# Optimization experiments

Hardware: AMD Instinct MI355X
Metric: run time of the kernel (lower is better)

The kernel has to match this reference:

```python
import jax, jax.numpy as jnp
import numpy as np

TOP_K = 9  # ATSSMatcher default


def setup_inputs() -> dict:
    key = jax.random.key(0)
    k1, k2, k3, k4 = jax.random.split(key, 4)
    N, M = 120000, 800
    IMG = 1024.0
    # anchors: valid x1<x2, y1<y2 boxes
    a_ctr = jax.random.uniform(k1, (N, 2)) * IMG
    a_sz = jax.random.uniform(k2, (N, 2)) * 60.0 + 8.0
    anchors = jnp.concatenate([a_ctr - a_sz / 2, a_ctr + a_sz / 2], axis=1)
    g_ctr = jax.random.uniform(k3, (M, 2)) * IMG
    g_sz = jax.random.uniform(k4, (M, 2)) * 100.0 + 10.0
    gt_boxes = jnp.concatenate([g_ctr - g_sz / 2, g_ctr + g_sz / 2], axis=1)
    return {"anchors": anchors, "gt_boxes": gt_boxes}


def _box_iou(a, b):
    # a: [N,4], b: [M,4] -> [N,M]
    area_a = (a[:, 2] - a[:, 0]) * (a[:, 3] - a[:, 1])
    area_b = (b[:, 2] - b[:, 0]) * (b[:, 3] - b[:, 1])
    lt = jnp.maximum(a[:, None, :2], b[None, :, :2])
    rb = jnp.minimum(a[:, None, 2:], b[None, :, 2:])
    wh = jnp.clip(rb - lt, 0.0)
    inter = wh[..., 0] * wh[..., 1]
    union = area_a[:, None] + area_b[None, :] - inter
    return inter / jnp.maximum(union, 1e-12)


def reference(anchors, gt_boxes):
    N = anchors.shape[0]
    M = gt_boxes.shape[0]
    ious = _box_iou(anchors, gt_boxes)                         # [N, M]
    a_ctr = (anchors[:, :2] + anchors[:, 2:]) / 2              # [N, 2]
    g_ctr = (gt_boxes[:, :2] + gt_boxes[:, 2:]) / 2            # [M, 2]
    # center distances [M, N] (per-GT rows for top-k along last axis)
    d = jnp.linalg.norm(a_ctr[None, :, :] - g_ctr[:, None, :], axis=-1)
    _, topk_idx = jax.lax.top_k(-d, TOP_K)                     # [M, TOP_K] nearest anchors
    topk_ious = jnp.take_along_axis(ious.T, topk_idx, axis=1)  # [M, TOP_K]
    iou_mean = topk_ious.mean(axis=1)                          # [M]
    iou_std = jnp.std(topk_ious, axis=1, ddof=1)               # torch .std() is unbiased
    thresh = iou_mean + iou_std                                # [M]
    candidate = ious >= thresh[None, :]                        # [N, M]
    cx, cy = a_ctr[:, 0], a_ctr[:, 1]
    inside = ((cx[:, None] >= gt_boxes[None, :, 0]) &
              (cx[:, None] <= gt_boxes[None, :, 2]) &
              (cy[:, None] >= gt_boxes[None, :, 1]) &
              (cy[:, None] <= gt_boxes[None, :, 3]))           # [N, M]
    pos = candidate & inside                                   # [N, M]
    gt_ids = jnp.arange(M, dtype=jnp.int32)[None, :]
    matched_idxs = jnp.max(jnp.where(pos, gt_ids, -1), axis=1)  # [N]
    gathered = jnp.take_along_axis(
        ious, jnp.clip(matched_idxs, 0)[:, None].astype(jnp.int32), axis=1)[:, 0]
    max_ious = jnp.where(matched_idxs >= 0, gathered, 0.0)
    return matched_idxs.astype(jnp.int64), max_ious
```

## Files before the change

kernel.cpp:

```cpp
#include <hip/hip_runtime.h>
#include <stdint.h>

typedef unsigned int u32;
typedef unsigned long long u64;

#define TOPK 9
#define GA 64
#define CELL_A 16.0f
#define NCA (GA * GA)
#define GG 16
#define CELL_G 64.0f
#define NCG (GG * GG)
#define CAPA 96
#define CAPG 160
#define OVA 8192
#define OVG 1024

__global__ __launch_bounds__(256) void zero_counts(u32* __restrict__ p, int n)
{
    int i = blockIdx.x * 256 + threadIdx.x;
    if (i < n) p[i] = 0u;
}

__global__ __launch_bounds__(256) void bucket_insert(
    const float4* __restrict__ a4, const float4* __restrict__ g4,
    u32* __restrict__ cursA, u32* __restrict__ cursG, u32* __restrict__ ovfCnt,
    float2* __restrict__ bkCtr, u32* __restrict__ bkIdx,
    u32* __restrict__ gtBkt,
    u32* __restrict__ ovAidx, float2* __restrict__ ovActr,
    u32* __restrict__ ovGidx, int N, int M)
{
    int gid = blockIdx.x * 256 + threadIdx.x;
    if (gid < N) {
        float4 a = a4[gid];
        float cx = (a.x + a.z) * 0.5f;
        float cy = (a.y + a.w) * 0.5f;
        int ix = min(GA - 1, max(0, (int)(cx * (1.0f / CELL_A))));
        int iy = min(GA - 1, max(0, (int)(cy * (1.0f / CELL_A))));
        int cell = iy * GA + ix;
        u32 p = atomicAdd(&cursA[cell], 1u);
        if (p < CAPA) {
            bkCtr[cell * CAPA + p] = make_float2(cx, cy);
            bkIdx[cell * CAPA + p] = (u32)gid;
        } else {
            u32 q = atomicAdd(&ovfCnt[0], 1u);
            if (q < OVA) { ovAidx[q] = (u32)gid; ovActr[q] = make_float2(cx, cy); }
        }
    } else if (gid < N + M) {
        int m = gid - N;
        float4 g = g4[m];
        int ix0 = min(GG - 1, max(0, (int)floorf(g.x * (1.0f / CELL_G))));
        int iy0 = min(GG - 1, max(0, (int)floorf(g.y * (1.0f / CELL_G))));
        int ix1 = min(GG - 1, max(0, (int)floorf(g.z * (1.0f / CELL_G))));
        int iy1 = min(GG - 1, max(0, (int)floorf(g.w * (1.0f / CELL_G))));
        for (int j = iy0; j <= iy1; ++j)
            for (int i = ix0; i <= ix1; ++i) {
                int cell = j * GG + i;
                u32 p = atomicAdd(&cursG[cell], 1u);
                if (p < CAPG) gtBkt[cell * CAPG + p] = (u32)m;
                else {
                    u32 q = atomicAdd(&ovfCnt[1], 1u);
                    if (q < OVG) ovGidx[q] = (u32)m;
                }
            }
    }
}

__global__ __launch_bounds__(256) void atss_query(
    const float4* __restrict__ a4, const float* __restrict__ gts,
    const u32* __restrict__ cursA, const float2* __restrict__ bkCtr,
    const u32* __restrict__ bkIdx, const u32* __restrict__ ovfCnt,
    const u32* __restrict__ ovAidx, const float2* __restrict__ ovActr,
    float* __restrict__ thresh, int N, int M)
{
    const int wid  = threadIdx.x >> 6;
    const int lane = threadIdx.x & 63;
    const int m = blockIdx.x * 4 + wid;
    if (m >= M) return;

    const float gx0 = gts[m * 4 + 0], gy0 = gts[m * 4 + 1];
    const float gx1 = gts[m * 4 + 2], gy1 = gts[m * 4 + 3];
    const float gcx = (gx0 + gx1) * 0.5f;
    const float gcy = (gy0 + gy1) * 0.5f;
    const int ci = min(GA - 1, max(0, (int)(gcx * (1.0f / CELL_A))));
    const int cj = min(GA - 1, max(0, (int)(gcy * (1.0f / CELL_A))));

    u32 cum = 0;
    float maxd2 = 0.f;
    for (int r = 0; r < GA && cum < TOPK; ++r) {
        int ncell = (r == 0) ? 1 : 8 * r;
        u32 myc = 0;
        float mymax = 0.f;
        for (int k = lane; k < ncell; k += 64) {
            int di = 0, dj = 0;
            if (r > 0) {
                int side = k / (2 * r), pos = k % (2 * r);
                if (side == 0)      { di = -r + pos; dj = -r; }
                else if (side == 1) { di = r;        dj = -r + pos; }
                else if (side == 2) { di = r - pos;  dj = r; }
                else                { di = -r;       dj = r - pos; }
            }
            int i = ci + di, j = cj + dj;
            if (i < 0 || i >= GA || j < 0 || j >= GA) continue;
            u32 cnt = cursA[j * GA + i];
            if (cnt) {
                myc += cnt;
                float x0 = i * CELL_A, x1 = x0 + CELL_A;
                float y0 = j * CELL_A, y1 = y0 + CELL_A;
                float dxm = fmaxf(gcx - x0, x1 - gcx);
                float dym = fmaxf(gcy - y0, y1 - gcy);
                mymax = fmaxf(mymax, dxm * dxm + dym * dym);
            }
        }
#pragma unroll
        for (int s2 = 1; s2 <= 32; s2 <<= 1) {
            myc += __shfl_xor(myc, s2, 64);
            mymax = fmaxf(mymax, __shfl_xor(mymax, s2, 64));
        }
        cum += myc;
        maxd2 = fmaxf(maxd2, mymax);
    }
    const float D2pad = maxd2 * 1.0001f + 1.0f;

    u64 kk[TOPK];
#pragma unroll
    for (int i = 0; i < TOPK; ++i) kk[i] = ~0ULL;

    const int rs = 1 + (int)(sqrtf(D2pad) * (1.0f / CELL_A));
    const int jlo = max(0, cj - rs), jhi = min(GA - 1, cj + rs);
    const int ilo = max(0, ci - rs), ihi = min(GA - 1, ci + rs);
    for (int j = jlo; j <= jhi; ++j) {
        float y0 = j * CELL_A, y1 = y0 + CELL_A;
        float mdy = fmaxf(fmaxf(y0 - gcy, gcy - y1), 0.f);
        for (int i = ilo; i <= ihi; ++i) {
            float x0 = i * CELL_A, x1 = x0 + CELL_A;
            float mdx = fmaxf(fmaxf(x0 - gcx, gcx - x1), 0.f);
            if (mdx * mdx + mdy * mdy > D2pad) continue;
            int c = j * GA + i;
            u32 cnt = min(cursA[c], (u32)CAPA);
            u32 base = (u32)c * CAPA;
            for (u32 tc = lane; tc < cnt; tc += 64) {
                u32 n = bkIdx[base + tc];
                float2 cc = bkCtr[base + tc];
                float ddx = cc.x - gcx, ddy = cc.y - gcy;
                float d2 = ddx * ddx + ddy * ddy;
                if (d2 <= D2pad) {
                    float d = sqrtf(d2);
                    u64 key = ((u64)__float_as_uint(d) << 32) | n;
                    if (key < kk[TOPK - 1]) {
                        u64 t2 = key;
#pragma unroll
                        for (int q = 0; q < TOPK; ++q) {
                            u64 lo = (kk[q] < t2) ? kk[q] : t2;
                            u64 hi = (kk[q] < t2) ? t2 : kk[q];
                            kk[q] = lo;
                            t2 = hi;
                        }
                    }
                }
            }
        }
    }
    {
        u32 nov = min(ovfCnt[0], (u32)OVA);
        for (u32 tc = lane; tc < nov; tc += 64) {
            u32 n = ovAidx[tc];
            float2 cc = ovActr[tc];
            float ddx = cc.x - gcx, ddy = cc.y - gcy;
            float d2 = ddx * ddx + ddy * ddy;
            if (d2 <= D2pad) {
                float d = sqrtf(d2);
                u64 key = ((u64)__float_as_uint(d) << 32) | n;
                if (key < kk[TOPK - 1]) {
                    u64 t2 = key;
#pragma unroll
                    for (int q = 0; q < TOPK; ++q) {
                        u64 lo = (kk[q] < t2) ? kk[q] : t2;
                        u64 hi = (kk[q] < t2) ? t2 : kk[q];
                        kk[q] = lo;
                        t2 = hi;
                    }
                }
            }
        }
    }

    u64 wins[TOPK];
#pragma unroll
    for (int rd = 0; rd < TOPK; ++rd) {
        u64 w = kk[0];
#pragma unroll
        for (int s2 = 1; s2 <= 32; s2 <<= 1) {
            u64 o = __shfl_xor(w, s2, 64);
            if (o < w) w = o;
        }
        wins[rd] = w;
        if (kk[0] == w) {
#pragma unroll
            for (int q = 0; q < TOPK - 1; ++q) kk[q] = kk[q + 1];
            kk[TOPK - 1] = ~0ULL;
        }
    }

    if (lane == 0) {
        const float area_g = (gx1 - gx0) * (gy1 - gy0);
        float vals[TOPK];
        float sum = 0.f;
#pragma unroll
        for (int r = 0; r < TOPK; ++r) {
            int idx = (int)(u32)(wins[r] & 0xffffffffULL);
            float4 a = a4[idx];
            float area_a = (a.z - a.x) * (a.w - a.y);
            float ltx = fmaxf(a.x, gx0), lty = fmaxf(a.y, gy0);
            float rbx = fminf(a.z, gx1), rby = fminf(a.w, gy1);
            float w2 = fmaxf(rbx - ltx, 0.f);
            float h2 = fmaxf(rby - lty, 0.f);
            float inter = w2 * h2;
            float uni = area_a + area_g - inter;
            float iou = inter / fmaxf(uni, 1e-12f);
            vals[r] = iou;
            sum += iou;
        }
        float mean = sum / 9.0f;
        float var = 0.f;
#pragma unroll
        for (int r = 0; r < TOPK; ++r) {
            float d2 = vals[r] - mean;
            var += d2 * d2;
        }
        float sd = sqrtf(var / 8.0f);
        thresh[m] = mean + sd;
    }
}

__global__ __launch_bounds__(256) void atss_assign(
    const float4* __restrict__ a4, const float4* __restrict__ g4,
    const float* __restrict__ thresh,
    const u32* __restrict__ cursG, const u32* __restrict__ gtBkt,
    const u32* __restrict__ ovfCnt, const u32* __restrict__ ovGidx,
    float* __restrict__ out_idx, float* __restrict__ out_iou, int N, int M)
{
    int n = blockIdx.x * 256 + threadIdx.x;
    if (n >= N) return;

    float4 a = a4[n];
    float area_a = (a.z - a.x) * (a.w - a.y);
    float cx = (a.x + a.z) * 0.5f;
    float cy = (a.y + a.w) * 0.5f;

    int ig = min(GG - 1, max(0, (int)(cx * (1.0f / CELL_G))));
    int jg = min(GG - 1, max(0, (int)(cy * (1.0f / CELL_G))));
    int cell = jg * GG + ig;

    u64 best = 0;
    u32 cnt = min(cursG[cell], (u32)CAPG);
    u32 base = (u32)cell * CAPG;
    for (u32 t2 = 0; t2 < cnt; ++t2) {
        int mi = (int)gtBkt[base + t2];
        float4 g = g4[mi];
        if (cx >= g.x && cx <= g.z && cy >= g.y && cy <= g.w) {
            float area_g = (g.z - g.x) * (g.w - g.y);
            float ltx = fmaxf(a.x, g.x), lty = fmaxf(a.y, g.y);
            float rbx = fminf(a.z, g.z), rby = fminf(a.w, g.w);
            float w = fmaxf(rbx - ltx, 0.f);
            float h = fmaxf(rby - lty, 0.f);
            float inter = w * h;
            float uni = area_a + area_g - inter;
            float iou = inter / fmaxf(uni, 1e-12f);
            if (iou >= thresh[mi]) {
                u64 cand = ((u64)(u32)(mi + 1) << 32) | __float_as_uint(iou);
                if (cand > best) best = cand;
            }
        }
    }
    {
        u32 nog = min(ovfCnt[1], (u32)OVG);
        for (u32 t2 = 0; t2 < nog; ++t2) {
            int mi = (int)ovGidx[t2];
            float4 g = g4[mi];
            if (cx >= g.x && cx <= g.z && cy >= g.y && cy <= g.w) {
                float area_g = (g.z - g.x) * (g.w - g.y);
                float ltx = fmaxf(a.x, g.x), lty = fmaxf(a.y, g.y);
                float rbx = fminf(a.z, g.z), rby = fminf(a.w, g.w);
                float w = fmaxf(rbx - ltx, 0.f);
                float h = fmaxf(rby - lty, 0.f);
                float inter = w * h;
                float uni = area_a + area_g - inter;
                float iou = inter / fmaxf(uni, 1e-12f);
                if (iou >= thresh[mi]) {
                    u64 cand = ((u64)(u32)(mi + 1) << 32) | __float_as_uint(iou);
                    if (cand > best) best = cand;
                }
            }
        }
    }

    int mm = (int)(best >> 32) - 1;
    out_idx[n] = (float)mm;
    out_iou[n] = (mm >= 0) ? __uint_as_float((u32)best) : 0.f;
}

__global__ __launch_bounds__(256) void fb_centers(
    const float4* __restrict__ a4, float2* __restrict__ c2, int N)
{
    int n = blockIdx.x * 256 + threadIdx.x;
    if (n < N) {
        float4 a = a4[n];
        c2[n] = make_float2((a.x + a.z) * 0.5f, (a.y + a.w) * 0.5f);
    }
}

__global__ __launch_bounds__(256) void fb_thresh(
    const float4* __restrict__ a4, const float2* __restrict__ c2,
    const float* __restrict__ gts, float* __restrict__ thresh, int N)
{
    const int m = blockIdx.x;
    const int tid = threadIdx.x;
    const float gx0 = gts[m * 4 + 0], gy0 = gts[m * 4 + 1];
    const float gx1 = gts[m * 4 + 2], gy1 = gts[m * 4 + 3];
    const float gcx = (gx0 + gx1) * 0.5f;
    const float gcy = (gy0 + gy1) * 0.5f;

    float vmin = __builtin_inff();
    for (int n = tid; n < N; n += 512) {
        float2 c = c2[n];
        float dx = c.x - gcx, dy = c.y - gcy;
        vmin = fminf(vmin, dx * dx + dy * dy);
    }
    float v = vmin, w = 0.f;
#pragma unroll
    for (int r = 0; r < TOPK; ++r) {
        float t = v;
#pragma unroll
        for (int s = 1; s <= 32; s <<= 1) t = fminf(t, __shfl_xor(t, s, 64));
        w = t;
        if (v == w) v = __builtin_inff();
    }
    const float T = sqrtf(w) * 1.0001f + 1e-6f;

    u64 k[TOPK];
#pragma unroll
    for (int i = 0; i < TOPK; ++i) k[i] = ~0ULL;
    for (int n = tid; n < N; n += 256) {
        float2 c = c2[n];
        float dx = c.x - gcx, dy = c.y - gcy;
        float d = sqrtf(dx * dx + dy * dy);
        if (d <= T) {
            u64 key = ((u64)__float_as_uint(d) << 32) | (unsigned)n;
            if (key < k[TOPK - 1]) {
                u64 t = key;
#pragma unroll
                for (int i = 0; i < TOPK; ++i) {
                    u64 lo = (k[i] < t) ? k[i] : t;
                    u64 hi = (k[i] < t) ? t : k[i];
                    k[i] = lo;
                    t = hi;
                }
            }
        }
    }
    __shared__ u64 red[256];
    __shared__ int top9[TOPK];
#pragma unroll 1
    for (int r = 0; r < TOPK; ++r) {
        red[tid] = k[0];
        __syncthreads();
        for (int s = 128; s > 0; s >>= 1) {
            if (tid < s) {
                u64 o = red[tid + s];
                if (o < red[tid]) red[tid] = o;
            }
            __syncthreads();
        }
        u64 win = red[0];
        if (tid == 0) top9[r] = (int)(unsigned)(win & 0xffffffffULL);
        __syncthreads();
        if (k[0] == win) {
#pragma unroll
            for (int i = 0; i < TOPK - 1; ++i) k[i] = k[i + 1];
            k[TOPK - 1] = ~0ULL;
        }
    }
    if (tid == 0) {
        const float area_g = (gx1 - gx0) * (gy1 - gy0);
        float vals[TOPK];
        float s = 0.f;
#pragma unroll
        for (int r = 0; r < TOPK; ++r) {
            float4 a = a4[top9[r]];
            float area_a = (a.z - a.x) * (a.w - a.y);
            float ltx = fmaxf(a.x, gx0), lty = fmaxf(a.y, gy0);
            float rbx = fminf(a.z, gx1), rby = fminf(a.w, gy1);
            float w2 = fmaxf(rbx - ltx, 0.f);
            float h2 = fmaxf(rby - lty, 0.f);
            float inter = w2 * h2;
            float uni = area_a + area_g - inter;
            float iou = inter / fmaxf(uni, 1e-12f);
            vals[r] = iou;
            s += iou;
        }
        float mean = s / 9.0f;
        float var = 0.f;
#pragma unroll
        for (int r = 0; r < TOPK; ++r) {
            float d2 = vals[r] - mean;
            var += d2 * d2;
        }
        thresh[m] = mean + sqrtf(var / 8.0f);
    }
}

__global__ __launch_bounds__(256) void fb_assign(
    const float4* __restrict__ a4, const float4* __restrict__ g4,
    const float* __restrict__ thresh,
    float* __restrict__ out_idx, float* __restrict__ out_iou, int N, int M)
{
    extern __shared__ char smem[];
    float4* sg = (float4*)smem;
    float2* se = (float2*)(smem + (size_t)M * 16);
    for (int i = threadIdx.x; i < M; i += 256) {
        float4 g = g4[i];
        sg[i] = g;
        se[i] = make_float2((g.z - g.x) * (g.w - g.y), thresh[i]);
    }
    __syncthreads();
    int n = blockIdx.x * 256 + threadIdx.x;
    if (n >= N) return;
    float4 a = a4[n];
    float area_a = (a.z - a.x) * (a.w - a.y);
    float cx = (a.x + a.z) * 0.5f;
    float cy = (a.y + a.w) * 0.5f;
    u64 best = 0;
    for (int mi = 0; mi < M; ++mi) {
        float4 g = sg[mi];
        if (cx >= g.x && cx <= g.z && cy >= g.y && cy <= g.w) {
            float2 e = se[mi];
            float ltx = fmaxf(a.x, g.x), lty = fmaxf(a.y, g.y);
            float rbx = fminf(a.z, g.z), rby = fminf(a.w, g.w);
            float w = fmaxf(rbx - ltx, 0.f);
            float h = fmaxf(rby - lty, 0.f);
            float inter = w * h;
            float uni = area_a + e.x - inter;
            float iou = inter / fmaxf(uni, 1e-12f);
            if (iou >= e.y)
                best = ((u64)(u32)(mi + 1) << 32) | __float_as_uint(iou);
        }
    }
    int mm = (int)(best >> 32) - 1;
    out_idx[n] = (float)mm;
    out_iou[n] = (mm >= 0) ? __uint_as_float((u32)best) : 0.f;
}

extern "C" void kernel_launch(void* const* d_in, const int* in_sizes, int n_in,
                              void* d_out, int out_size, void* d_ws, size_t ws_size,
                              hipStream_t stream) {
    const float4* a4 = (const float4*)d_in[0];
    const float4* g4 = (const float4*)d_in[1];
    const float* gts = (const float*)d_in[1];
    const int N = in_sizes[0] / 4;
    const int M = in_sizes[1] / 4;

    const size_t oCursA  = 0;
    const size_t oCursG  = oCursA + NCA;
    const size_t oOvfCnt = oCursG + NCG;
    const size_t oThresh = oOvfCnt + 2;
    size_t oBkCtr = oThresh + (size_t)M;
    oBkCtr = (oBkCtr + 1) & ~(size_t)1;
    const size_t oBkIdx  = oBkCtr + 2 * (size_t)NCA * CAPA;
    const size_t oGtBkt  = oBkIdx + (size_t)NCA * CAPA;
    const size_t oOvAidx = oGtBkt + (size_t)NCG * CAPG;
    size_t oOvActr = oOvAidx + OVA;
    oOvActr = (oOvActr + 1) & ~(size_t)1;
    const size_t oOvGidx = oOvActr + 2 * (size_t)OVA;
    const size_t needBytes = (oOvGidx + OVG) * sizeof(u32);

    if (ws_size >= needBytes) {
        u32* w = (u32*)d_ws;
        u32* cursA    = w + oCursA;
        u32* cursG    = w + oCursG;
        u32* ovfCnt   = w + oOvfCnt;
        float* thr    = (float*)(w + oThresh);
        float2* bkCtr = (float2*)(w + oBkCtr);
        u32* bkIdx    = w + oBkIdx;
        u32* gtBkt    = w + oGtBkt;
        u32* ovAidx   = w + oOvAidx;
        float2* ovActr= (float2*)(w + oOvActr);
        u32* ovGidx   = w + oOvGidx;

        const int nZero = NCA + NCG + 2;
        zero_counts<<<(nZero + 255) / 256, 256, 0, stream>>>(cursA, nZero);
        bucket_insert<<<(N + M + 255) / 256, 256, 0, stream>>>(
            a4, g4, cursA, cursG, ovfCnt, bkCtr, bkIdx, gtBkt,
            ovAidx, ovActr, ovGidx, N, M);
        atss_query<<<(M + 3) / 4, 256, 0, stream>>>(
            a4, gts, cursA, bkCtr, bkIdx, ovfCnt, ovAidx, ovActr, thr, N, M);
        atss_assign<<<(N + 255) / 256, 256, 0, stream>>>(
            a4, g4, thr, cursG, gtBkt, ovfCnt, ovGidx,
            (float*)d_out, (float*)d_out + N, N, M);
    } else {
        float* thr = (float*)d_ws;
        float2* centers = (float2*)d_out;
        fb_centers<<<(N + 255) / 256, 256, 0, stream>>>(a4, centers, N);
        fb_thresh<<<M, 256, 0, stream>>>(a4, (const float2*)centers, gts, thr, N);
        size_t lds = (size_t)M * 24;
        fb_assign<<<(N + 255) / 256, 256, lds, stream>>>(
            a4, g4, thr, (float*)d_out, (float*)d_out + N, N, M);
    }
}
```

Baseline: 53.58 us.

## Fuse bucketing, threshold query and assignment into one cooperative kernel

Replaces four separate launches (zero, bucket insert, per-GT query, per-anchor assign) with one cooperative kernel. Phases are separated by grid-wide syncs and use grid-stride loops, to remove launch overhead and inter-kernel gaps. In exchange it adds three grid barriers. The single kernel carries the union of all phases' register pressure, which can lower occupancy in the memory-bound assign phase. The launch return code is not checked.

```diff
diff --git a/kernel.cpp b/kernel.cpp
--- a/kernel.cpp
+++ b/kernel.cpp
@@ -1,5 +1,8 @@
 #include <hip/hip_runtime.h>
+#include <hip/hip_cooperative_groups.h>
 #include <stdint.h>
+
+namespace cg = cooperative_groups;
 
 typedef unsigned int u32;
 typedef unsigned long long u64;
@@ -16,275 +19,268 @@
 #define OVA 8192
 #define OVG 1024
 
-__global__ __launch_bounds__(256) void zero_counts(u32* __restrict__ p, int n)
+__global__ __launch_bounds__(256) void atss_fused(
+    const float4* __restrict__ a4, const float4* __restrict__ g4,
+    u32* __restrict__ w, float* __restrict__ outp, int N, int M)
 {
-    int i = blockIdx.x * 256 + threadIdx.x;
-    if (i < n) p[i] = 0u;
-}
-
-__global__ __launch_bounds__(256) void bucket_insert(
-    const float4* __restrict__ a4, const float4* __restrict__ g4,
-    u32* __restrict__ cursA, u32* __restrict__ cursG, u32* __restrict__ ovfCnt,
-    float2* __restrict__ bkCtr, u32* __restrict__ bkIdx,
-    u32* __restrict__ gtBkt,
-    u32* __restrict__ ovAidx, float2* __restrict__ ovActr,
-    u32* __restrict__ ovGidx, int N, int M)
-{
-    int gid = blockIdx.x * 256 + threadIdx.x;
-    if (gid < N) {
-        float4 a = a4[gid];
+    cg::grid_group grid = cg::this_grid();
+
+    const size_t oCursA  = 0;
+    const size_t oCursG  = oCursA + NCA;
+    const size_t oOvfCnt = oCursG + NCG;
+    const size_t oThresh = oOvfCnt + 2;
+    size_t oBkCtr = oThresh + (size_t)M;
+    oBkCtr = (oBkCtr + 1) & ~(size_t)1;
+    const size_t oBkIdx  = oBkCtr + 2 * (size_t)NCA * CAPA;
+    const size_t oGtBkt  = oBkIdx + (size_t)NCA * CAPA;
+    const size_t oOvAidx = oGtBkt + (size_t)NCG * CAPG;
+    size_t oOvActr = oOvAidx + OVA;
+    oOvActr = (oOvActr + 1) & ~(size_t)1;
+    const size_t oOvGidx = oOvActr + 2 * (size_t)OVA;
+
+    u32* cursA     = w + oCursA;
+    u32* cursG     = w + oCursG;
+    u32* ovfCnt    = w + oOvfCnt;
+    float* thresh  = (float*)(w + oThresh);
+    float2* bkCtr  = (float2*)(w + oBkCtr);
+    u32* bkIdx     = w + oBkIdx;
+    u32* gtBkt     = w + oGtBkt;
+    u32* ovAidx    = w + oOvAidx;
+    float2* ovActr = (float2*)(w + oOvActr);
+    u32* ovGidx    = w + oOvGidx;
+    const float* gts = (const float*)g4;
+    float* out_idx = outp;
+    float* out_iou = outp + N;
+
+    const int gtid = blockIdx.x * 256 + (int)threadIdx.x;
+    const int gstride = (int)gridDim.x * 256;
+
+    for (int i = gtid; i < NCA + NCG + 2; i += gstride) w[i] = 0u;
+
+    grid.sync();
+
+    for (int gid = gtid; gid < N + M; gid += gstride) {
+        if (gid < N) {
+            float4 a = a4[gid];
+            float cx = (a.x + a.z) * 0.5f;
+            float cy = (a.y + a.w) * 0.5f;
+            int ix = min(GA - 1, max(0, (int)(cx * (1.0f / CELL_A))));
+            int iy = min(GA - 1, max(0, (int)(cy * (1.0f / CELL_A))));
+            int cell = iy * GA + ix;
+            u32 p = atomicAdd(&cursA[cell], 1u);
+            if (p < CAPA) {
+                bkCtr[cell * CAPA + p] = make_float2(cx, cy);
+                bkIdx[cell * CAPA + p] = (u32)gid;
+            } else {
+                u32 q = atomicAdd(&ovfCnt[0], 1u);
+                if (q < OVA) { ovAidx[q] = (u32)gid; ovActr[q] = make_float2(cx, cy); }
+            }
+        } else {
+            int m = gid - N;
+            float4 g = g4[m];
+            int ix0 = min(GG - 1, max(0, (int)floorf(g.x * (1.0f / CELL_G))));
+            int iy0 = min(GG - 1, max(0, (int)floorf(g.y * (1.0f / CELL_G))));
+            int ix1 = min(GG - 1, max(0, (int)floorf(g.z * (1.0f / CELL_G))));
+            int iy1 = min(GG - 1, max(0, (int)floorf(g.w * (1.0f / CELL_G))));
+            for (int j = iy0; j <= iy1; ++j)
+                for (int i = ix0; i <= ix1; ++i) {
+                    int cell = j * GG + i;
+                    u32 p = atomicAdd(&cursG[cell], 1u);
+                    if (p < CAPG) gtBkt[cell * CAPG + p] = (u32)m;
+                    else {
+                        u32 q = atomicAdd(&ovfCnt[1], 1u);
+                        if (q < OVG) ovGidx[q] = (u32)m;
+                    }
+                }
+        }
+    }
+
+    grid.sync();
+
+    {
+        const int lane = threadIdx.x & 63;
+        for (int m = (gtid >> 6); m < M; m += (gstride >> 6)) {
+            const float gx0 = gts[m * 4 + 0], gy0 = gts[m * 4 + 1];
+            const float gx1 = gts[m * 4 + 2], gy1 = gts[m * 4 + 3];
+            const float gcx = (gx0 + gx1) * 0.5f;
+            const float gcy = (gy0 + gy1) * 0.5f;
+            const int ci = min(GA - 1, max(0, (int)(gcx * (1.0f / CELL_A))));
+            const int cj = min(GA - 1, max(0, (int)(gcy * (1.0f / CELL_A))));
+
+            u32 cum = 0;
+            float maxd2 = 0.f;
+            for (int r = 0; r < GA && cum < TOPK; ++r) {
+                int ncell = (r == 0) ? 1 : 8 * r;
+                u32 myc = 0;
+                float mymax = 0.f;
+                for (int k = lane; k < ncell; k += 64) {
+                    int di = 0, dj = 0;
+                    if (r > 0) {
+                        int side = k / (2 * r), pos = k % (2 * r);
+                        if (side == 0)      { di = -r + pos; dj = -r; }
+                        else if (side == 1) { di = r;        dj = -r + pos; }
+                        else if (side == 2) { di = r - pos;  dj = r; }
+                        else                { di = -r;       dj = r - pos; }
+                    }
+                    int i = ci + di, j = cj + dj;
+                    if (i < 0 || i >= GA || j < 0 || j >= GA) continue;
+                    u32 cnt = cursA[j * GA + i];
+                    if (cnt) {
+                        myc += cnt;
+                        float x0 = i * CELL_A, x1 = x0 + CELL_A;
+                        float y0 = j * CELL_A, y1 = y0 + CELL_A;
+                        float dxm = fmaxf(gcx - x0, x1 - gcx);
+                        float dym = fmaxf(gcy - y0, y1 - gcy);
+                        mymax = fmaxf(mymax, dxm * dxm + dym * dym);
+                    }
+                }
+#pragma unroll
+                for (int s2 = 1; s2 <= 32; s2 <<= 1) {
+                    myc += __shfl_xor(myc, s2, 64);
+                    mymax = fmaxf(mymax, __shfl_xor(mymax, s2, 64));
+                }
+                cum += myc;
+                maxd2 = fmaxf(maxd2, mymax);
+            }
+            const float D2pad = maxd2 * 1.0001f + 1.0f;
+
+            u64 kk[TOPK];
+#pragma unroll
+            for (int i = 0; i < TOPK; ++i) kk[i] = ~0ULL;
+
+            const int rs = 1 + (int)(sqrtf(D2pad) * (1.0f / CELL_A));
+            const int jlo = max(0, cj - rs), jhi = min(GA - 1, cj + rs);
+            const int ilo = max(0, ci - rs), ihi = min(GA - 1, ci + rs);
+            for (int j = jlo; j <= jhi; ++j) {
+                float y0 = j * CELL_A, y1 = y0 + CELL_A;
+                float mdy = fmaxf(fmaxf(y0 - gcy, gcy - y1), 0.f);
+                for (int i = ilo; i <= ihi; ++i) {
+                    float x0 = i * CELL_A, x1 = x0 + CELL_A;
+                    float mdx = fmaxf(fmaxf(x0 - gcx, gcx - x1), 0.f);
+                    if (mdx * mdx + mdy * mdy > D2pad) continue;
+                    int c = j * GA + i;
+                    u32 cnt = min(cursA[c], (u32)CAPA);
+                    u32 base = (u32)c * CAPA;
+                    for (u32 tc = lane; tc < cnt; tc += 64) {
+                        u32 n = bkIdx[base + tc];
+                        float2 cc = bkCtr[base + tc];
+                        float ddx = cc.x - gcx, ddy = cc.y - gcy;
+                        float d2 = ddx * ddx + ddy * ddy;
+                        if (d2 <= D2pad) {
+                            float d = sqrtf(d2);
+                            u64 key = ((u64)__float_as_uint(d) << 32) | n;
+                            if (key < kk[TOPK - 1]) {
+                                u64 t2 = key;
+#pragma unroll
+                                for (int q = 0; q < TOPK; ++q) {
+                                    u64 lo = (kk[q] < t2) ? kk[q] : t2;
+                                    u64 hi = (kk[q] < t2) ? t2 : kk[q];
+                                    kk[q] = lo;
+                                    t2 = hi;
+                                }
+                            }
+                        }
+                    }
+                }
+            }
+            {
+                u32 nov = min(ovfCnt[0], (u32)OVA);
+                for (u32 tc = lane; tc < nov; tc += 64) {
+                    u32 n = ovAidx[tc];
+                    float2 cc = ovActr[tc];
+                    float ddx = cc.x - gcx, ddy = cc.y - gcy;
+                    float d2 = ddx * ddx + ddy * ddy;
+                    if (d2 <= D2pad) {
+                        float d = sqrtf(d2);
+                        u64 key = ((u64)__float_as_uint(d) << 32) | n;
+                        if (key < kk[TOPK - 1]) {
+                            u64 t2 = key;
+#pragma unroll
+                            for (int q = 0; q < TOPK; ++q) {
+                                u64 lo = (kk[q] < t2) ? kk[q] : t2;
+                                u64 hi = (kk[q] < t2) ? t2 : kk[q];
+                                kk[q] = lo;
+                                t2 = hi;
+                            }
+                        }
+                    }
+                }
+            }
+
+            u64 wins[TOPK];
+#pragma unroll
+            for (int rd = 0; rd < TOPK; ++rd) {
+                u64 wv = kk[0];
+#pragma unroll
+                for (int s2 = 1; s2 <= 32; s2 <<= 1) {
+                    u64 o = __shfl_xor(wv, s2, 64);
+                    if (o < wv) wv = o;
+                }
+                wins[rd] = wv;
+                if (kk[0] == wv) {
+#pragma unroll
+                    for (int q = 0; q < TOPK - 1; ++q) kk[q] = kk[q + 1];
+                    kk[TOPK - 1] = ~0ULL;
+                }
+            }
+
+            if (lane == 0) {
+                const float area_g = (gx1 - gx0) * (gy1 - gy0);
+                float vals[TOPK];
+                float sum = 0.f;
+#pragma unroll
+                for (int r = 0; r < TOPK; ++r) {
+                    int idx = (int)(u32)(wins[r] & 0xffffffffULL);
+                    float4 a = a4[idx];
+                    float area_a = (a.z - a.x) * (a.w - a.y);
+                    float ltx = fmaxf(a.x, gx0), lty = fmaxf(a.y, gy0);
+                    float rbx = fminf(a.z, gx1), rby = fminf(a.w, gy1);
+                    float w2 = fmaxf(rbx - ltx, 0.f);
+                    float h2 = fmaxf(rby - lty, 0.f);
+                    float inter = w2 * h2;
+                    float uni = area_a + area_g - inter;
+                    float iou = inter / fmaxf(uni, 1e-12f);
+                    vals[r] = iou;
+                    sum += iou;
+                }
+                float mean = sum / 9.0f;
+                float var = 0.f;
+#pragma unroll
+                for (int r = 0; r < TOPK; ++r) {
+                    float d2 = vals[r] - mean;
+                    var += d2 * d2;
+                }
+                float sd = sqrtf(var / 8.0f);
+                thresh[m] = mean + sd;
+            }
+        }
+    }
+
+    grid.sync();
+
+    for (int n = gtid; n < N; n += gstride) {
+        float4 a = a4[n];
+        float area_a = (a.z - a.x) * (a.w - a.y);
         float cx = (a.x + a.z) * 0.5f;
         float cy = (a.y + a.w) * 0.5f;
-        int ix = min(GA - 1, max(0, (int)(cx * (1.0f / CELL_A))));
-        int iy = min(GA - 1, max(0, (int)(cy * (1.0f / CELL_A))));
-        int cell = iy * GA + ix;
-        u32 p = atomicAdd(&cursA[cell], 1u);
-        if (p < CAPA) {
-            bkCtr[cell * CAPA + p] = make_float2(cx, cy);
-            bkIdx[cell * CAPA + p] = (u32)gid;
-        } else {
-            u32 q = atomicAdd(&ovfCnt[0], 1u);
-            if (q < OVA) { ovAidx[q] = (u32)gid; ovActr[q] = make_float2(cx, cy); }
-        }
-    } else if (gid < N + M) {
-        int m = gid - N;
-        float4 g = g4[m];
-        int ix0 = min(GG - 1, max(0, (int)floorf(g.x * (1.0f / CELL_G))));
-        int iy0 = min(GG - 1, max(0, (int)floorf(g.y * (1.0f / CELL_G))));
-        int ix1 = min(GG - 1, max(0, (int)floorf(g.z * (1.0f / CELL_G))));
-        int iy1 = min(GG - 1, max(0, (int)floorf(g.w * (1.0f / CELL_G))));
-        for (int j = iy0; j <= iy1; ++j)
-            for (int i = ix0; i <= ix1; ++i) {
-                int cell = j * GG + i;
-                u32 p = atomicAdd(&cursG[cell], 1u);
-                if (p < CAPG) gtBkt[cell * CAPG + p] = (u32)m;
-                else {
-                    u32 q = atomicAdd(&ovfCnt[1], 1u);
-                    if (q < OVG) ovGidx[q] = (u32)m;
-                }
-            }
-    }
-}
-
-__global__ __launch_bounds__(256) void atss_query(
-    const float4* __restrict__ a4, const float* __restrict__ gts,
-    const u32* __restrict__ cursA, const float2* __restrict__ bkCtr,
-    const u32* __restrict__ bkIdx, const u32* __restrict__ ovfCnt,
-    const u32* __restrict__ ovAidx, const float2* __restrict__ ovActr,
-    float* __restrict__ thresh, int N, int M)
-{
-    const int wid  = threadIdx.x >> 6;
-    const int lane = threadIdx.x & 63;
-    const int m = blockIdx.x * 4 + wid;
-    if (m >= M) return;
-
-    const float gx0 = gts[m * 4 + 0], gy0 = gts[m * 4 + 1];
-    const float gx1 = gts[m * 4 + 2], gy1 = gts[m * 4 + 3];
-    const float gcx = (gx0 + gx1) * 0.5f;
-    const float gcy = (gy0 + gy1) * 0.5f;
-    const int ci = min(GA - 1, max(0, (int)(gcx * (1.0f / CELL_A))));
-    const int cj = min(GA - 1, max(0, (int)(gcy * (1.0f / CELL_A))));
-
-    u32 cum = 0;
-    float maxd2 = 0.f;
-    for (int r = 0; r < GA && cum < TOPK; ++r) {
-        int ncell = (r == 0) ? 1 : 8 * r;
-        u32 myc = 0;
-        float mymax = 0.f;
-        for (int k = lane; k < ncell; k += 64) {
-            int di = 0, dj = 0;
-            if (r > 0) {
-                int side = k / (2 * r), pos = k % (2 * r);
-                if (side == 0)      { di = -r + pos; dj = -r; }
-                else if (side == 1) { di = r;        dj = -r + pos; }
-                else if (side == 2) { di = r - pos;  dj = r; }
-                else                { di = -r;       dj = r - pos; }
-            }
-            int i = ci + di, j = cj + dj;
-            if (i < 0 || i >= GA || j < 0 || j >= GA) continue;
-            u32 cnt = cursA[j * GA + i];
-            if (cnt) {
-                myc += cnt;
-                float x0 = i * CELL_A, x1 = x0 + CELL_A;
-                float y0 = j * CELL_A, y1 = y0 + CELL_A;
-                float dxm = fmaxf(gcx - x0, x1 - gcx);
-                float dym = fmaxf(gcy - y0, y1 - gcy);
-                mymax = fmaxf(mymax, dxm * dxm + dym * dym);
-            }
-        }
-#pragma unroll
-        for (int s2 = 1; s2 <= 32; s2 <<= 1) {
-            myc += __shfl_xor(myc, s2, 64);
-            mymax = fmaxf(mymax, __shfl_xor(mymax, s2, 64));
-        }
-        cum += myc;
-        maxd2 = fmaxf(maxd2, mymax);
-    }
-    const float D2pad = maxd2 * 1.0001f + 1.0f;
-
-    u64 kk[TOPK];
-#pragma unroll
-    for (int i = 0; i < TOPK; ++i) kk[i] = ~0ULL;
-
-    const int rs = 1 + (int)(sqrtf(D2pad) * (1.0f / CELL_A));
-    const int jlo = max(0, cj - rs), jhi = min(GA - 1, cj + rs);
-    const int ilo = max(0, ci - rs), ihi = min(GA - 1, ci + rs);
-    for (int j = jlo; j <= jhi; ++j) {
-        float y0 = j * CELL_A, y1 = y0 + CELL_A;
-        float mdy = fmaxf(fmaxf(y0 - gcy, gcy - y1), 0.f);
-        for (int i = ilo; i <= ihi; ++i) {
-            float x0 = i * CELL_A, x1 = x0 + CELL_A;
-            float mdx = fmaxf(fmaxf(x0 - gcx, gcx - x1), 0.f);
-            if (mdx * mdx + mdy * mdy > D2pad) continue;
-            int c = j * GA + i;
-            u32 cnt = min(cursA[c], (u32)CAPA);
-            u32 base = (u32)c * CAPA;
-            for (u32 tc = lane; tc < cnt; tc += 64) {
-                u32 n = bkIdx[base + tc];
-                float2 cc = bkCtr[base + tc];
-                float ddx = cc.x - gcx, ddy = cc.y - gcy;
-                float d2 = ddx * ddx + ddy * ddy;
-                if (d2 <= D2pad) {
-                    float d = sqrtf(d2);
-                    u64 key = ((u64)__float_as_uint(d) << 32) | n;
-                    if (key < kk[TOPK - 1]) {
-                        u64 t2 = key;
-#pragma unroll
-                        for (int q = 0; q < TOPK; ++q) {
-                            u64 lo = (kk[q] < t2) ? kk[q] : t2;
-                            u64 hi = (kk[q] < t2) ? t2 : kk[q];
-                            kk[q] = lo;
-                            t2 = hi;
-                        }
-                    }
-                }
-            }
-        }
-    }
-    {
-        u32 nov = min(ovfCnt[0], (u32)OVA);
-        for (u32 tc = lane; tc < nov; tc += 64) {
-            u32 n = ovAidx[tc];
-            float2 cc = ovActr[tc];
-            float ddx = cc.x - gcx, ddy = cc.y - gcy;
-            float d2 = ddx * ddx + ddy * ddy;
-            if (d2 <= D2pad) {
-                float d = sqrtf(d2);
-                u64 key = ((u64)__float_as_uint(d) << 32) | n;
-                if (key < kk[TOPK - 1]) {
-                    u64 t2 = key;
-#pragma unroll
-                    for (int q = 0; q < TOPK; ++q) {
-                        u64 lo = (kk[q] < t2) ? kk[q] : t2;
-                        u64 hi = (kk[q] < t2) ? t2 : kk[q];
-                        kk[q] = lo;
-                        t2 = hi;
-                    }
-                }
-            }
-        }
-    }
-
-    u64 wins[TOPK];
-#pragma unroll
-    for (int rd = 0; rd < TOPK; ++rd) {
-        u64 w = kk[0];
-#pragma unroll
-        for (int s2 = 1; s2 <= 32; s2 <<= 1) {
-            u64 o = __shfl_xor(w, s2, 64);
-            if (o < w) w = o;
-        }
-        wins[rd] = w;
-        if (kk[0] == w) {
-#pragma unroll
-            for (int q = 0; q < TOPK - 1; ++q) kk[q] = kk[q + 1];
-            kk[TOPK - 1] = ~0ULL;
-        }
-    }
-
-    if (lane == 0) {
-        const float area_g = (gx1 - gx0) * (gy1 - gy0);
-        float vals[TOPK];
-        float sum = 0.f;
-#pragma unroll
-        for (int r = 0; r < TOPK; ++r) {
-            int idx = (int)(u32)(wins[r] & 0xffffffffULL);
-            float4 a = a4[idx];
-            float area_a = (a.z - a.x) * (a.w - a.y);
-            float ltx = fmaxf(a.x, gx0), lty = fmaxf(a.y, gy0);
-            float rbx = fminf(a.z, gx1), rby = fminf(a.w, gy1);
-            float w2 = fmaxf(rbx - ltx, 0.f);
-            float h2 = fmaxf(rby - lty, 0.f);
-            float inter = w2 * h2;
-            float uni = area_a + area_g - inter;
-            float iou = inter / fmaxf(uni, 1e-12f);
-            vals[r] = iou;
-            sum += iou;
-        }
-        float mean = sum / 9.0f;
-        float var = 0.f;
-#pragma unroll
-        for (int r = 0; r < TOPK; ++r) {
-            float d2 = vals[r] - mean;
-            var += d2 * d2;
-        }
-        float sd = sqrtf(var / 8.0f);
-        thresh[m] = mean + sd;
-    }
-}
-
-__global__ __launch_bounds__(256) void atss_assign(
-    const float4* __restrict__ a4, const float4* __restrict__ g4,
-    const float* __restrict__ thresh,
-    const u32* __restrict__ cursG, const u32* __restrict__ gtBkt,
-    const u32* __restrict__ ovfCnt, const u32* __restrict__ ovGidx,
-    float* __restrict__ out_idx, float* __restrict__ out_iou, int N, int M)
-{
-    int n = blockIdx.x * 256 + threadIdx.x;
-    if (n >= N) return;
-
-    float4 a = a4[n];
-    float area_a = (a.z - a.x) * (a.w - a.y);
-    float cx = (a.x + a.z) * 0.5f;
-    float cy = (a.y + a.w) * 0.5f;
-
-    int ig = min(GG - 1, max(0, (int)(cx * (1.0f / CELL_G))));
-    int jg = min(GG - 1, max(0, (int)(cy * (1.0f / CELL_G))));
-    int cell = jg * GG + ig;
-
-    u64 best = 0;
-    u32 cnt = min(cursG[cell], (u32)CAPG);
-    u32 base = (u32)cell * CAPG;
-    for (u32 t2 = 0; t2 < cnt; ++t2) {
-        int mi = (int)gtBkt[base + t2];
-        float4 g = g4[mi];
-        if (cx >= g.x && cx <= g.z && cy >= g.y && cy <= g.w) {
-            float area_g = (g.z - g.x) * (g.w - g.y);
-            float ltx = fmaxf(a.x, g.x), lty = fmaxf(a.y, g.y);
-            float rbx = fminf(a.z, g.z), rby = fminf(a.w, g.w);
-            float w = fmaxf(rbx - ltx, 0.f);
-            float h = fmaxf(rby - lty, 0.f);
-            float inter = w * h;
-            float uni = area_a + area_g - inter;
-            float iou = inter / fmaxf(uni, 1e-12f);
-            if (iou >= thresh[mi]) {
-                u64 cand = ((u64)(u32)(mi + 1) << 32) | __float_as_uint(iou);
-                if (cand > best) best = cand;
-            }
-        }
-    }
-    {
-        u32 nog = min(ovfCnt[1], (u32)OVG);
-        for (u32 t2 = 0; t2 < nog; ++t2) {
-            int mi = (int)ovGidx[t2];
+
+        int ig = min(GG - 1, max(0, (int)(cx * (1.0f / CELL_G))));
+        int jg = min(GG - 1, max(0, (int)(cy * (1.0f / CELL_G))));
+        int cell = jg * GG + ig;
+
+        u64 best = 0;
+        u32 cnt = min(cursG[cell], (u32)CAPG);
+        u32 base = (u32)cell * CAPG;
+        for (u32 t2 = 0; t2 < cnt; ++t2) {
+            int mi = (int)gtBkt[base + t2];
             float4 g = g4[mi];
             if (cx >= g.x && cx <= g.z && cy >= g.y && cy <= g.w) {
                 float area_g = (g.z - g.x) * (g.w - g.y);
                 float ltx = fmaxf(a.x, g.x), lty = fmaxf(a.y, g.y);
                 float rbx = fminf(a.z, g.z), rby = fminf(a.w, g.w);
-                float w = fmaxf(rbx - ltx, 0.f);
-                float h = fmaxf(rby - lty, 0.f);
-                float inter = w * h;
+                float ww = fmaxf(rbx - ltx, 0.f);
+                float hh = fmaxf(rby - lty, 0.f);
+                float inter = ww * hh;
                 float uni = area_a + area_g - inter;
                 float iou = inter / fmaxf(uni, 1e-12f);
                 if (iou >= thresh[mi]) {
@@ -293,11 +289,32 @@
                 }
             }
         }
-    }
-
-    int mm = (int)(best >> 32) - 1;
-    out_idx[n] = (float)mm;
-    out_iou[n] = (mm >= 0) ? __uint_as_float((u32)best) : 0.f;
+        {
+            u32 nog = min(ovfCnt[1], (u32)OVG);
+            for (u32 t2 = 0; t2 < nog; ++t2) {
+                int mi = (int)ovGidx[t2];
+                float4 g = g4[mi];
+                if (cx >= g.x && cx <= g.z && cy >= g.y && cy <= g.w) {
+                    float area_g = (g.z - g.x) * (g.w - g.y);
+                    float ltx = fmaxf(a.x, g.x), lty = fmaxf(a.y, g.y);
+                    float rbx = fminf(a.z, g.z), rby = fminf(a.w, g.w);
+                    float ww = fmaxf(rbx - ltx, 0.f);
+                    float hh = fmaxf(rby - lty, 0.f);
+                    float inter = ww * hh;
+                    float uni = area_a + area_g - inter;
+                    float iou = inter / fmaxf(uni, 1e-12f);
+                    if (iou >= thresh[mi]) {
+                        u64 cand = ((u64)(u32)(mi + 1) << 32) | __float_as_uint(iou);
+                        if (cand > best) best = cand;
+                    }
+                }
+            }
+        }
+
+        int mm = (int)(best >> 32) - 1;
+        out_idx[n] = (float)mm;
+        out_iou[n] = (mm >= 0) ? __uint_as_float((u32)best) : 0.f;
+    }
 }
 
 __global__ __launch_bounds__(256) void fb_centers(
@@ -457,8 +474,8 @@
     const float4* a4 = (const float4*)d_in[0];
     const float4* g4 = (const float4*)d_in[1];
     const float* gts = (const float*)d_in[1];
-    const int N = in_sizes[0] / 4;
-    const int M = in_sizes[1] / 4;
+    int N = in_sizes[0] / 4;
+    int M = in_sizes[1] / 4;
 
     const size_t oCursA  = 0;
     const size_t oCursG  = oCursA + NCA;
@@ -476,27 +493,15 @@
 
     if (ws_size >= needBytes) {
         u32* w = (u32*)d_ws;
-        u32* cursA    = w + oCursA;
-        u32* cursG    = w + oCursG;
-        u32* ovfCnt   = w + oOvfCnt;
-        float* thr    = (float*)(w + oThresh);
-        float2* bkCtr = (float2*)(w + oBkCtr);
-        u32* bkIdx    = w + oBkIdx;
-        u32* gtBkt    = w + oGtBkt;
-        u32* ovAidx   = w + oOvAidx;
-        float2* ovActr= (float2*)(w + oOvActr);
-        u32* ovGidx   = w + oOvGidx;
-
-        const int nZero = NCA + NCG + 2;
-        zero_counts<<<(nZero + 255) / 256, 256, 0, stream>>>(cursA, nZero);
-        bucket_insert<<<(N + M + 255) / 256, 256, 0, stream>>>(
-            a4, g4, cursA, cursG, ovfCnt, bkCtr, bkIdx, gtBkt,
-            ovAidx, ovActr, ovGidx, N, M);
-        atss_query<<<(M + 3) / 4, 256, 0, stream>>>(
-            a4, gts, cursA, bkCtr, bkIdx, ovfCnt, ovAidx, ovActr, thr, N, M);
-        atss_assign<<<(N + 255) / 256, 256, 0, stream>>>(
-            a4, g4, thr, cursG, gtBkt, ovfCnt, ovGidx,
-            (float*)d_out, (float*)d_out + N, N, M);
+        float* outf = (float*)d_out;
+        int nblk = (N + M + 255) / 256;
+        int qblk = (M + 3) / 4;
+        if (qblk > nblk) nblk = qblk;
+        void* args[] = { (void*)&a4, (void*)&g4, (void*)&w, (void*)&outf,
+                         (void*)&N, (void*)&M };
+        hipLaunchCooperativeKernel((const void*)atss_fused,
+                                   dim3((unsigned)nblk), dim3(256),
+                                   args, 0, stream);
     } else {
         float* thr = (float*)d_ws;
         float2* centers = (float2*)d_out;
```

Measured after the change: 192.0 us. +258.3%, slower.

## Use a full block per GT in ATSS query and pack bucket slots as float4

Applied to the files above, without the earlier changes.

The top-k query now assigns a whole 256-thread block to each GT box instead of one wavefront. The four waves scan ring counts and candidate cells in parallel and merge their partial top-9 lists through shared memory. Anchor bucket entries are packed into a single float4 (center plus index), and GT boxes are copied into their grid buckets so the assign kernel skips an indirect gather. This trades extra block-level synchronisation and larger workspace writes for more parallelism and fewer dependent loads.

```diff
diff --git a/kernel.cpp b/kernel.cpp
--- a/kernel.cpp
+++ b/kernel.cpp
@@ -25,7 +25,7 @@
 __global__ __launch_bounds__(256) void bucket_insert(
     const float4* __restrict__ a4, const float4* __restrict__ g4,
     u32* __restrict__ cursA, u32* __restrict__ cursG, u32* __restrict__ ovfCnt,
-    float2* __restrict__ bkCtr, u32* __restrict__ bkIdx,
+    float4* __restrict__ slotA, float4* __restrict__ gtBox,
     u32* __restrict__ gtBkt,
     u32* __restrict__ ovAidx, float2* __restrict__ ovActr,
     u32* __restrict__ ovGidx, int N, int M)
@@ -40,8 +40,8 @@
         int cell = iy * GA + ix;
         u32 p = atomicAdd(&cursA[cell], 1u);
         if (p < CAPA) {
-            bkCtr[cell * CAPA + p] = make_float2(cx, cy);
-            bkIdx[cell * CAPA + p] = (u32)gid;
+            slotA[cell * CAPA + p] =
+                make_float4(cx, cy, __uint_as_float((u32)gid), 0.f);
         } else {
             u32 q = atomicAdd(&ovfCnt[0], 1u);
             if (q < OVA) { ovAidx[q] = (u32)gid; ovActr[q] = make_float2(cx, cy); }
@@ -57,8 +57,10 @@
             for (int i = ix0; i <= ix1; ++i) {
                 int cell = j * GG + i;
                 u32 p = atomicAdd(&cursG[cell], 1u);
-                if (p < CAPG) gtBkt[cell * CAPG + p] = (u32)m;
-                else {
+                if (p < CAPG) {
+                    gtBox[cell * CAPG + p] = g;
+                    gtBkt[cell * CAPG + p] = (u32)m;
+                } else {
                     u32 q = atomicAdd(&ovfCnt[1], 1u);
                     if (q < OVG) ovGidx[q] = (u32)m;
                 }
@@ -68,15 +70,20 @@
 
 __global__ __launch_bounds__(256) void atss_query(
     const float4* __restrict__ a4, const float* __restrict__ gts,
-    const u32* __restrict__ cursA, const float2* __restrict__ bkCtr,
-    const u32* __restrict__ bkIdx, const u32* __restrict__ ovfCnt,
+    const u32* __restrict__ cursA, const float4* __restrict__ slotA,
+    const u32* __restrict__ ovfCnt,
     const u32* __restrict__ ovAidx, const float2* __restrict__ ovActr,
-    float* __restrict__ thresh, int N, int M)
-{
-    const int wid  = threadIdx.x >> 6;
-    const int lane = threadIdx.x & 63;
-    const int m = blockIdx.x * 4 + wid;
+    float* __restrict__ thresh, int M)
+{
+    const int m = blockIdx.x;
     if (m >= M) return;
+    const int tid  = (int)threadIdx.x;
+    const int wid  = tid >> 6;
+    const int lane = tid & 63;
+
+    __shared__ u32   s_cnt[4];
+    __shared__ float s_max[4];
+    __shared__ u64   s_top[4 * TOPK];
 
     const float gx0 = gts[m * 4 + 0], gy0 = gts[m * 4 + 1];
     const float gx1 = gts[m * 4 + 2], gy1 = gts[m * 4 + 3];
@@ -85,10 +92,9 @@
     const int ci = min(GA - 1, max(0, (int)(gcx * (1.0f / CELL_A))));
     const int cj = min(GA - 1, max(0, (int)(gcy * (1.0f / CELL_A))));
 
-    u32 cum = 0;
-    float maxd2 = 0.f;
-    for (int r = 0; r < GA && cum < TOPK; ++r) {
-        int ncell = (r == 0) ? 1 : 8 * r;
+    {
+        const int r = wid;
+        const int ncell = (r == 0) ? 1 : 8 * r;
         u32 myc = 0;
         float mymax = 0.f;
         for (int k = lane; k < ncell; k += 64) {
@@ -117,8 +123,51 @@
             myc += __shfl_xor(myc, s2, 64);
             mymax = fmaxf(mymax, __shfl_xor(mymax, s2, 64));
         }
-        cum += myc;
-        maxd2 = fmaxf(maxd2, mymax);
+        if (lane == 0) { s_cnt[wid] = myc; s_max[wid] = mymax; }
+    }
+    __syncthreads();
+
+    u32 cum = 0;
+    float maxd2 = 0.f;
+#pragma unroll
+    for (int r = 0; r < 4; ++r) {
+        if (cum < TOPK) {
+            cum += s_cnt[r];
+            maxd2 = fmaxf(maxd2, s_max[r]);
+        }
+    }
+    if (cum < TOPK) {
+        for (int r = 4; r < GA && cum < TOPK; ++r) {
+            const int ncell = 8 * r;
+            u32 myc = 0;
+            float mymax = 0.f;
+            for (int k = lane; k < ncell; k += 64) {
+                int side = k / (2 * r), pos = k % (2 * r);
+                int di, dj;
+                if (side == 0)      { di = -r + pos; dj = -r; }
+                else if (side == 1) { di = r;        dj = -r + pos; }
+                else if (side == 2) { di = r - pos;  dj = r; }
+                else                { di = -r;       dj = r - pos; }
+                int i = ci + di, j = cj + dj;
+                if (i < 0 || i >= GA || j < 0 || j >= GA) continue;
+                u32 cnt = cursA[j * GA + i];
+                if (cnt) {
+                    myc += cnt;
+                    float x0 = i * CELL_A, x1 = x0 + CELL_A;
+                    float y0 = j * CELL_A, y1 = y0 + CELL_A;
+                    float dxm = fmaxf(gcx - x0, x1 - gcx);
+                    float dym = fmaxf(gcy - y0, y1 - gcy);
+                    mymax = fmaxf(mymax, dxm * dxm + dym * dym);
+                }
+            }
+#pragma unroll
+            for (int s2 = 1; s2 <= 32; s2 <<= 1) {
+                myc += __shfl_xor(myc, s2, 64);
+                mymax = fmaxf(mymax, __shfl_xor(mymax, s2, 64));
+            }
+            cum += myc;
+            maxd2 = fmaxf(maxd2, mymax);
+        }
     }
     const float D2pad = maxd2 * 1.0001f + 1.0f;
 
@@ -129,33 +178,34 @@
     const int rs = 1 + (int)(sqrtf(D2pad) * (1.0f / CELL_A));
     const int jlo = max(0, cj - rs), jhi = min(GA - 1, cj + rs);
     const int ilo = max(0, ci - rs), ihi = min(GA - 1, ci + rs);
-    for (int j = jlo; j <= jhi; ++j) {
+    const int ncols  = ihi - ilo + 1;
+    const int ncells = (jhi - jlo + 1) * ncols;
+    for (int t = wid; t < ncells; t += 4) {
+        int j = jlo + t / ncols;
+        int i = ilo + t % ncols;
         float y0 = j * CELL_A, y1 = y0 + CELL_A;
         float mdy = fmaxf(fmaxf(y0 - gcy, gcy - y1), 0.f);
-        for (int i = ilo; i <= ihi; ++i) {
-            float x0 = i * CELL_A, x1 = x0 + CELL_A;
-            float mdx = fmaxf(fmaxf(x0 - gcx, gcx - x1), 0.f);
-            if (mdx * mdx + mdy * mdy > D2pad) continue;
-            int c = j * GA + i;
-            u32 cnt = min(cursA[c], (u32)CAPA);
-            u32 base = (u32)c * CAPA;
-            for (u32 tc = lane; tc < cnt; tc += 64) {
-                u32 n = bkIdx[base + tc];
-                float2 cc = bkCtr[base + tc];
-                float ddx = cc.x - gcx, ddy = cc.y - gcy;
-                float d2 = ddx * ddx + ddy * ddy;
-                if (d2 <= D2pad) {
-                    float d = sqrtf(d2);
-                    u64 key = ((u64)__float_as_uint(d) << 32) | n;
-                    if (key < kk[TOPK - 1]) {
-                        u64 t2 = key;
-#pragma unroll
-                        for (int q = 0; q < TOPK; ++q) {
-                            u64 lo = (kk[q] < t2) ? kk[q] : t2;
-                            u64 hi = (kk[q] < t2) ? t2 : kk[q];
-                            kk[q] = lo;
-                            t2 = hi;
-                        }
+        float x0 = i * CELL_A, x1 = x0 + CELL_A;
+        float mdx = fmaxf(fmaxf(x0 - gcx, gcx - x1), 0.f);
+        if (mdx * mdx + mdy * mdy > D2pad) continue;
+        int c = j * GA + i;
+        u32 cnt = min(cursA[c], (u32)CAPA);
+        u32 base = (u32)c * CAPA;
+        for (u32 tc = lane; tc < cnt; tc += 64) {
+            float4 s = slotA[base + tc];
+            float ddx = s.x - gcx, ddy = s.y - gcy;
+            float d2 = ddx * ddx + ddy * ddy;
+            if (d2 <= D2pad) {
+                float d = sqrtf(d2);
+                u64 key = ((u64)__float_as_uint(d) << 32) | __float_as_uint(s.z);
+                if (key < kk[TOPK - 1]) {
+                    u64 t2 = key;
+#pragma unroll
+                    for (int q = 0; q < TOPK; ++q) {
+                        u64 lo = (kk[q] < t2) ? kk[q] : t2;
+                        u64 hi = (kk[q] < t2) ? t2 : kk[q];
+                        kk[q] = lo;
+                        t2 = hi;
                     }
                 }
             }
@@ -163,7 +213,7 @@
     }
     {
         u32 nov = min(ovfCnt[0], (u32)OVA);
-        for (u32 tc = lane; tc < nov; tc += 64) {
+        for (u32 tc = (u32)tid; tc < nov; tc += 256) {
             u32 n = ovAidx[tc];
             float2 cc = ovActr[tc];
             float ddx = cc.x - gcx, ddy = cc.y - gcy;
@@ -185,58 +235,78 @@
         }
     }
 
-    u64 wins[TOPK];
-#pragma unroll
-    for (int rd = 0; rd < TOPK; ++rd) {
-        u64 w = kk[0];
-#pragma unroll
-        for (int s2 = 1; s2 <= 32; s2 <<= 1) {
-            u64 o = __shfl_xor(w, s2, 64);
-            if (o < w) w = o;
-        }
-        wins[rd] = w;
-        if (kk[0] == w) {
-#pragma unroll
-            for (int q = 0; q < TOPK - 1; ++q) kk[q] = kk[q + 1];
-            kk[TOPK - 1] = ~0ULL;
-        }
-    }
-
-    if (lane == 0) {
-        const float area_g = (gx1 - gx0) * (gy1 - gy0);
-        float vals[TOPK];
-        float sum = 0.f;
-#pragma unroll
-        for (int r = 0; r < TOPK; ++r) {
-            int idx = (int)(u32)(wins[r] & 0xffffffffULL);
-            float4 a = a4[idx];
-            float area_a = (a.z - a.x) * (a.w - a.y);
-            float ltx = fmaxf(a.x, gx0), lty = fmaxf(a.y, gy0);
-            float rbx = fminf(a.z, gx1), rby = fminf(a.w, gy1);
-            float w2 = fmaxf(rbx - ltx, 0.f);
-            float h2 = fmaxf(rby - lty, 0.f);
-            float inter = w2 * h2;
-            float uni = area_a + area_g - inter;
-            float iou = inter / fmaxf(uni, 1e-12f);
-            vals[r] = iou;
-            sum += iou;
-        }
-        float mean = sum / 9.0f;
-        float var = 0.f;
-#pragma unroll
-        for (int r = 0; r < TOPK; ++r) {
-            float d2 = vals[r] - mean;
-            var += d2 * d2;
-        }
-        float sd = sqrtf(var / 8.0f);
-        thresh[m] = mean + sd;
+    {
+        u64 wv;
+#pragma unroll
+        for (int rd = 0; rd < TOPK; ++rd) {
+            wv = kk[0];
+#pragma unroll
+            for (int s2 = 1; s2 <= 32; s2 <<= 1) {
+                u64 o = __shfl_xor(wv, s2, 64);
+                if (o < wv) wv = o;
+            }
+            if (lane == 0) s_top[wid * TOPK + rd] = wv;
+            if (kk[0] == wv) {
+#pragma unroll
+                for (int q = 0; q < TOPK - 1; ++q) kk[q] = kk[q + 1];
+                kk[TOPK - 1] = ~0ULL;
+            }
+        }
+    }
+    __syncthreads();
+
+    if (wid == 0) {
+        u64 v = (lane < 4 * TOPK) ? s_top[lane] : ~0ULL;
+        u64 wins[TOPK];
+#pragma unroll
+        for (int rd = 0; rd < TOPK; ++rd) {
+            u64 wv = v;
+#pragma unroll
+            for (int s2 = 1; s2 <= 32; s2 <<= 1) {
+                u64 o = __shfl_xor(wv, s2, 64);
+                if (o < wv) wv = o;
+            }
+            wins[rd] = wv;
+            if (v == wv) v = ~0ULL;
+        }
+
+        if (lane == 0) {
+            const float area_g = (gx1 - gx0) * (gy1 - gy0);
+            float vals[TOPK];
+            float sum = 0.f;
+#pragma unroll
+            for (int r = 0; r < TOPK; ++r) {
+                int idx = (int)(u32)(wins[r] & 0xffffffffULL);
+                float4 a = a4[idx];
+                float area_a = (a.z - a.x) * (a.w - a.y);
+                float ltx = fmaxf(a.x, gx0), lty = fmaxf(a.y, gy0);
+                float rbx = fminf(a.z, gx1), rby = fminf(a.w, gy1);
+                float w2 = fmaxf(rbx - ltx, 0.f);
+                float h2 = fmaxf(rby - lty, 0.f);
+                float inter = w2 * h2;
+                float uni = area_a + area_g - inter;
+                float iou = inter / fmaxf(uni, 1e-12f);
+                vals[r] = iou;
+                sum += iou;
+            }
+            float mean = sum / 9.0f;
+            float var = 0.f;
+#pragma unroll
+            for (int r = 0; r < TOPK; ++r) {
+                float d2 = vals[r] - mean;
+                var += d2 * d2;
+            }
+            float sd = sqrtf(var / 8.0f);
+            thresh[m] = mean + sd;
+        }
     }
 }
 
 __global__ __launch_bounds__(256) void atss_assign(
     const float4* __restrict__ a4, const float4* __restrict__ g4,
     const float* __restrict__ thresh,
-    const u32* __restrict__ cursG, const u32* __restrict__ gtBkt,
+    const u32* __restrict__ cursG, const float4* __restrict__ gtBox,
+    const u32* __restrict__ gtBkt,
     const u32* __restrict__ ovfCnt, const u32* __restrict__ ovGidx,
     float* __restrict__ out_idx, float* __restrict__ out_iou, int N, int M)
 {
@@ -256,9 +326,9 @@
     u32 cnt = min(cursG[cell], (u32)CAPG);
     u32 base = (u32)cell * CAPG;
     for (u32 t2 = 0; t2 < cnt; ++t2) {
-        int mi = (int)gtBkt[base + t2];
-        float4 g = g4[mi];
+        float4 g = gtBox[base + t2];
         if (cx >= g.x && cx <= g.z && cy >= g.y && cy <= g.w) {
+            int mi = (int)gtBkt[base + t2];
             float area_g = (g.z - g.x) * (g.w - g.y);
             float ltx = fmaxf(a.x, g.x), lty = fmaxf(a.y, g.y);
             float rbx = fminf(a.z, g.z), rby = fminf(a.w, g.w);
@@ -464,10 +534,10 @@
     const size_t oCursG  = oCursA + NCA;
     const size_t oOvfCnt = oCursG + NCG;
     const size_t oThresh = oOvfCnt + 2;
-    size_t oBkCtr = oThresh + (size_t)M;
-    oBkCtr = (oBkCtr + 1) & ~(size_t)1;
-    const size_t oBkIdx  = oBkCtr + 2 * (size_t)NCA * CAPA;
-    const size_t oGtBkt  = oBkIdx + (size_t)NCA * CAPA;
+    size_t oSlotA = oThresh + (size_t)M;
+    oSlotA = (oSlotA + 3) & ~(size_t)3;
+    const size_t oGtBox  = oSlotA + 4 * (size_t)NCA * CAPA;
+    const size_t oGtBkt  = oGtBox + 4 * (size_t)NCG * CAPG;
     const size_t oOvAidx = oGtBkt + (size_t)NCG * CAPG;
     size_t oOvActr = oOvAidx + OVA;
     oOvActr = (oOvActr + 1) & ~(size_t)1;
@@ -480,8 +550,8 @@
         u32* cursG    = w + oCursG;
         u32* ovfCnt   = w + oOvfCnt;
         float* thr    = (float*)(w + oThresh);
-        float2* bkCtr = (float2*)(w + oBkCtr);
-        u32* bkIdx    = w + oBkIdx;
+        float4* slotA = (float4*)(w + oSlotA);
+        float4* gtBox = (float4*)(w + oGtBox);
         u32* gtBkt    = w + oGtBkt;
         u32* ovAidx   = w + oOvAidx;
         float2* ovActr= (float2*)(w + oOvActr);
@@ -490,12 +560,12 @@
         const int nZero = NCA + NCG + 2;
         zero_counts<<<(nZero + 255) / 256, 256, 0, stream>>>(cursA, nZero);
         bucket_insert<<<(N + M + 255) / 256, 256, 0, stream>>>(
-            a4, g4, cursA, cursG, ovfCnt, bkCtr, bkIdx, gtBkt,
+            a4, g4, cursA, cursG, ovfCnt, slotA, gtBox, gtBkt,
             ovAidx, ovActr, ovGidx, N, M);
-        atss_query<<<(M + 3) / 4, 256, 0, stream>>>(
-            a4, gts, cursA, bkCtr, bkIdx, ovfCnt, ovAidx, ovActr, thr, N, M);
+        atss_query<<<M, 256, 0, stream>>>(
+            a4, gts, cursA, slotA, ovfCnt, ovAidx, ovActr, thr, M);
         atss_assign<<<(N + 255) / 256, 256, 0, stream>>>(
-            a4, g4, thr, cursG, gtBkt, ovfCnt, ovGidx,
+            a4, g4, thr, cursG, gtBox, gtBkt, ovfCnt, ovGidx,
             (float*)d_out, (float*)d_out + N, N, M);
     } else {
         float* thr = (float*)d_ws;
```

New measurement: 49.71 us. 1.08x faster.
